# Performance work log

Measured on AMD Instinct MI355X. Metric: run time of the kernel, lower is better.

Reference implementation:

```python
import jax, jax.numpy as jnp
import numpy as np

B, C, H, W = 32, 256, 64, 64
LN_EPS = 1e-5

def _conv1x1(x, w, b=None):
    # x: (b,c,h,w), w: (out,c) -> (b,out,h,w)
    y = jnp.einsum('bchw,oc->bohw', x, w)
    if b is not None:
        y = y + b[None, :, None, None]
    return y

def _hsigmoid(t):
    # mmcv HSigmoid: clamp((x + 3) / 6, 0, 1)
    return jnp.clip((t + 3.0) / 6.0, 0.0, 1.0)

def setup_inputs() -> dict:
    key = jax.random.key(0)
    ks = jax.random.split(key, 12)
    s = 0.05
    return {
        'x': jax.random.normal(ks[0], (B, C, H, W), jnp.float32),
        'conv0_w': jax.random.normal(ks[1], (C // 2, C), jnp.float32) * s,
        'conv0_b': jnp.zeros((C // 2,), jnp.float32),
        'bn1_w': jax.random.normal(ks[2], (C, C // 2), jnp.float32) * s,
        'bn1_b': jnp.zeros((C,), jnp.float32),
        'conv1_w': jax.random.normal(ks[3], (1, C), jnp.float32) * s,
        'conv1_b': jnp.zeros((1,), jnp.float32),
        'ln_g': jnp.ones((C,), jnp.float32),
        'ln_b': jnp.zeros((C,), jnp.float32),
        'sk_w1': jax.random.normal(ks[4], (C // 2, C), jnp.float32) * s,
        'sk_w2': jax.random.normal(ks[5], (C, C // 2), jnp.float32) * s,
        'res_w': jax.random.normal(ks[6], (C, C), jnp.float32) * s,
        'res_b': jnp.zeros((C,), jnp.float32),
    }

def reference(x, conv0_w, conv0_b, bn1_w, bn1_b, conv1_w, conv1_b,
              ln_g, ln_b, sk_w1, sk_w2, res_w, res_b):
    b, c, h, w = x.shape
    # ---- channel attention ----
    ca = _conv1x1(x, conv0_w, conv0_b)               # (b, c/2, h, w)
    ca = ca.mean(axis=(2, 3), keepdims=True)          # GAP -> (b, c/2, 1, 1)
    ca = _conv1x1(ca, bn1_w, bn1_b)                   # (b, c, 1, 1)
    ca = _hsigmoid(ca)
    v = ca.reshape(b, c)                              # nchw_to_nlc -> (b, 1, c); LN over c
    mu = v.mean(axis=-1, keepdims=True)
    var = ((v - mu) ** 2).mean(axis=-1, keepdims=True)
    v = (v - mu) * jax.lax.rsqrt(var + LN_EPS) * ln_g + ln_b
    ca = v.reshape(b, c, 1, 1)
    # ---- spatial attention ----
    sa = _conv1x1(x, conv1_w, conv1_b)                # (b, 1, h, w)
    # ---- parallel attention ----
    par = _hsigmoid(sa + ca)                          # (b, c, h, w)
    # ---- sequence attention: bmm outer product (b,c,1)x(b,1,hw) ----
    seq = _hsigmoid(ca * sa)                          # (b, c, h, w)
    # ---- SK module ----
    u = (seq + par).mean(axis=(2, 3), keepdims=True)  # GAP -> (b, c, 1, 1)
    u = _conv1x1(u, sk_w1)                            # (b, c/2, 1, 1), no bias
    u = _conv1x1(u, sk_w2)                            # (b, c, 1, 1), no bias
    a = jax.nn.softmax(u, axis=1)
    sk = seq * a + par * (1.0 - a)
    # softmax over spatial (nchw_to_nlc + Softmax(dim=1))
    sk = jax.nn.softmax(sk.reshape(b, c, h * w), axis=2).reshape(b, c, h, w)
    selected = x * sk
    # ---- self attention ----
    self_attn = selected.sum(axis=(2, 3)).reshape(b, c, 1, 1) + _conv1x1(x, res_w, res_b)
    return selected + self_attn
```

## Files before the change

### kernel.cpp

```cpp
#include <hip/hip_runtime.h>
#include <math.h>

#define B_  32
#define C_  256
#define HW_ 4096
#define LN_EPS 1e-5f

typedef __attribute__((ext_vector_type(4))) float f32x4;
typedef __attribute__((ext_vector_type(8))) short bf16x8;

__device__ __forceinline__ float hsig(float v) {
    return fminf(fmaxf((v + 3.0f) * (1.0f / 6.0f), 0.0f), 1.0f);
}
__device__ __forceinline__ float tval(float ca, float a, float sav) {
    return a * hsig(ca * sav) + (1.0f - a) * hsig(ca + sav);
}
__device__ __forceinline__ unsigned short f2bf(float f) {
    unsigned u = __float_as_uint(f);
    unsigned r = (u + 0x7fffu + ((u >> 16) & 1u)) >> 16;
    return (unsigned short)r;
}
__device__ __forceinline__ float bf2f(unsigned short h) {
    return __uint_as_float(((unsigned)h) << 16);
}

__global__ void k_pass1(const float* __restrict__ x, const float* __restrict__ w1,
                        float* __restrict__ sa,
                        float* __restrict__ xs_part)
{
    int tid = threadIdx.x, wave = tid >> 6, lane = tid & 63;
    int hwq = blockIdx.x, b = blockIdx.y, ct = blockIdx.z;
    int c0 = ct * 32;
    int hw0 = hwq * 1024;
    const float* xb = x + (size_t)b * (C_ * HW_) + hw0 + tid * 4;
    __shared__ float part[32 * 4];
    f32x4 sacc = {0.f, 0.f, 0.f, 0.f};
    #pragma unroll 4
    for (int cc = 0; cc < 32; ++cc) {
        int c = c0 + cc;
        f32x4 v = *(const f32x4*)(xb + (size_t)c * HW_);
        float wv = w1[c];
        sacc += wv * v;
        float h = (v.x + v.y) + (v.z + v.w);
        h += __shfl_xor(h, 32); h += __shfl_xor(h, 16); h += __shfl_xor(h, 8);
        h += __shfl_xor(h, 4);  h += __shfl_xor(h, 2);  h += __shfl_xor(h, 1);
        if (lane == 0) part[cc * 4 + wave] = h;
    }
    float* sp = sa + (size_t)b * HW_ + hw0 + tid * 4;
    atomicAdd(sp + 0, sacc.x);
    atomicAdd(sp + 1, sacc.y);
    atomicAdd(sp + 2, sacc.z);
    atomicAdd(sp + 3, sacc.w);
    __syncthreads();
    if (tid < 32)
        xs_part[((size_t)hwq * B_ + b) * C_ + c0 + tid] =
            part[tid * 4 + 0] + part[tid * 4 + 1] + part[tid * 4 + 2] + part[tid * 4 + 3];
}

__global__ void k_ca(const float* __restrict__ xs_part, const float* __restrict__ w0,
                     const float* __restrict__ b0, const float* __restrict__ w1,
                     const float* __restrict__ b1, const float* __restrict__ g,
                     const float* __restrict__ be, float* __restrict__ ca,
                     const float* __restrict__ rw, unsigned short* __restrict__ wbs) {
    int b = blockIdx.x, tid = threadIdx.x;
    __shared__ float xm[C_], t0[128], red[4];
    float xs = xs_part[((size_t)0 * B_ + b) * C_ + tid]
             + xs_part[((size_t)1 * B_ + b) * C_ + tid]
             + xs_part[((size_t)2 * B_ + b) * C_ + tid]
             + xs_part[((size_t)3 * B_ + b) * C_ + tid];
    xm[tid] = xs * (1.0f / HW_);
    __syncthreads();
    if (tid < 128) {
        float s = b0[tid];
        const float* wr = w0 + tid * C_;
        for (int c = 0; c < C_; ++c) s += wr[c] * xm[c];
        t0[tid] = s;
    }
    __syncthreads();
    float s = b1[tid];
    const float* wr = w1 + tid * 128;
    for (int o = 0; o < 128; ++o) s += wr[o] * t0[o];
    float v = hsig(s);
    float sum = v;
    #pragma unroll
    for (int o = 32; o; o >>= 1) sum += __shfl_xor(sum, o);
    if ((tid & 63) == 0) red[tid >> 6] = sum;
    __syncthreads();
    float mu = (red[0] + red[1] + red[2] + red[3]) * (1.0f / C_);
    __syncthreads();
    float d = v - mu;
    float sq = d * d;
    #pragma unroll
    for (int o = 32; o; o >>= 1) sq += __shfl_xor(sq, o);
    if ((tid & 63) == 0) red[tid >> 6] = sq;
    __syncthreads();
    float var = (red[0] + red[1] + red[2] + red[3]) * (1.0f / C_);
    ca[b * C_ + tid] = d * (1.0f / sqrtf(var + LN_EPS)) * g[tid] + be[tid];

    int gid = b * 256 + tid;
    int lane = gid & 63;
    int mi = (gid >> 6) & 3;
    int ks = (gid >> 8) & 7;
    int wv2 = gid >> 11;
    int m = wv2 * 64 + mi * 16 + (lane & 15);
    int kb = ks * 32 + (lane >> 4) * 8;
    const float* src = rw + m * C_ + kb;
    f32x4 a4 = *(const f32x4*)src;
    f32x4 b4 = *(const f32x4*)(src + 4);
    ushort4 o0 = { f2bf(a4.x), f2bf(a4.y), f2bf(a4.z), f2bf(a4.w) };
    ushort4 o1 = { f2bf(b4.x), f2bf(b4.y), f2bf(b4.z), f2bf(b4.w) };
    unsigned short* dst = wbs + (size_t)gid * 8;
    *(ushort4*)dst = o0;
    *(ushort4*)(dst + 4) = o1;
}

__global__ void k_u(const float* __restrict__ sa, const float* __restrict__ ca,
                    const float* __restrict__ b1, float* __restrict__ u) {
    int bc = blockIdx.x;
    int b = bc >> 8;
    int tid = threadIdx.x;
    float cav = ca[bc];
    float bias = b1[0];
    const float* sp = sa + (size_t)b * HW_;
    float s = 0.f;
    for (int i = 0; i < 16; ++i) {
        f32x4 v = *(const f32x4*)(sp + i * 256 + tid * 4);
        #pragma unroll
        for (int j = 0; j < 4; ++j) {
            float sv = v[j] + bias;
            s += hsig(cav * sv) + hsig(cav + sv);
        }
    }
    #pragma unroll
    for (int o = 32; o; o >>= 1) s += __shfl_xor(s, o);
    if (tid == 0) u[bc] = s * (1.0f / HW_);
}

__global__ void k_a(const float* __restrict__ u, const float* __restrict__ w1,
                    const float* __restrict__ w2, float* __restrict__ aout) {
    int b = blockIdx.x, tid = threadIdx.x;
    __shared__ float uu[C_], v0[128], red[4];
    uu[tid] = u[b * C_ + tid];
    __syncthreads();
    if (tid < 128) {
        float s = 0.f;
        const float* wr = w1 + tid * C_;
        for (int c = 0; c < C_; ++c) s += wr[c] * uu[c];
        v0[tid] = s;
    }
    __syncthreads();
    float s = 0.f;
    const float* wr = w2 + tid * 128;
    for (int o = 0; o < 128; ++o) s += wr[o] * v0[o];
    float m = s;
    #pragma unroll
    for (int o = 32; o; o >>= 1) m = fmaxf(m, __shfl_xor(m, o));
    if ((tid & 63) == 0) red[tid >> 6] = m;
    __syncthreads();
    m = fmaxf(fmaxf(red[0], red[1]), fmaxf(red[2], red[3]));
    __syncthreads();
    float e = __expf(s - m);
    float se = e;
    #pragma unroll
    for (int o = 32; o; o >>= 1) se += __shfl_xor(se, o);
    if ((tid & 63) == 0) red[tid >> 6] = se;
    __syncthreads();
    float tot = red[0] + red[1] + red[2] + red[3];
    aout[b * C_ + tid] = e / tot;
}

__global__ void k_stats(const float* __restrict__ x, const float* __restrict__ sa,
                        const float* __restrict__ b1,
                        const float* __restrict__ ca, const float* __restrict__ aw,
                        const float* __restrict__ res_b, f32x4* __restrict__ st4) {
    int bc = blockIdx.x;
    int b = bc >> 8, c = bc & 255;
    int tid = threadIdx.x;
    float cav = ca[bc], av = aw[bc];
    float bias = b1[0];
    const float* sp = sa + (size_t)b * HW_;
    const float* xp = x + (size_t)bc * HW_;
    float se = 0.f, xe = 0.f;
    #pragma unroll
    for (int i = 0; i < 4; ++i) {
        f32x4 s4 = *(const f32x4*)(sp + i * 1024 + tid * 4);
        f32x4 x4 = *(const f32x4*)(xp + i * 1024 + tid * 4);
        #pragma unroll
        for (int j = 0; j < 4; ++j) {
            float e = __expf(tval(cav, av, s4[j] + bias));
            se += e;
            xe += x4[j] * e;
        }
    }
    __shared__ float red[4], red2[4];
    #pragma unroll
    for (int o = 32; o; o >>= 1) { se += __shfl_xor(se, o); xe += __shfl_xor(xe, o); }
    if ((tid & 63) == 0) { red[tid >> 6] = se; red2[tid >> 6] = xe; }
    __syncthreads();
    if (tid == 0) {
        float S = red[0] + red[1] + red[2] + red[3];
        float X = red2[0] + red2[1] + red2[2] + red2[3];
        float rcp = 1.0f / S;
        f32x4 st = { cav, av, rcp, X * rcp + res_b[c] };
        st4[bc] = st;
    }
}

__global__ __launch_bounds__(256, 2) void k_out(
    const float* __restrict__ x, const unsigned short* __restrict__ wbs,
    const float* __restrict__ sa, const float* __restrict__ b1,
    const f32x4* __restrict__ st4, float* __restrict__ out)
{
    __shared__ __align__(16) unsigned short Bs[64 * 256];
    __shared__ f32x4 sst[C_];
    __shared__ float ssa[64];

    int b = blockIdx.x, tile = blockIdx.y;
    int n0 = tile * 64;
    int tid = threadIdx.x;
    int w = tid >> 6, lane = tid & 63;

    const float* xb = x + (size_t)b * (C_ * HW_);

    bf16x8 af[8][4];
    #pragma unroll
    for (int ks = 0; ks < 8; ++ks)
        #pragma unroll
        for (int mi = 0; mi < 4; ++mi)
            af[ks][mi] = *(const bf16x8*)(wbs + (size_t)(((w * 8 + ks) * 4 + mi) * 64 + lane) * 8);

    sst[tid] = st4[b * C_ + tid];
    if (tid < 64) ssa[tid] = sa[(size_t)b * HW_ + n0 + tid] + b1[0];

    #pragma unroll
    for (int p2 = 0; p2 < 8; ++p2) {
        int id = p2 * 256 + tid;
        int kp = id >> 4;
        int tcn = id & 15;
        const float* g0 = xb + (size_t)(2 * kp) * HW_ + n0 + 4 * tcn;
        f32x4 v0 = *(const f32x4*)g0;
        f32x4 v1 = *(const f32x4*)(g0 + HW_);
        #pragma unroll
        for (int i = 0; i < 4; ++i) {
            int n = 4 * tcn + i;
            unsigned val = (unsigned)f2bf(v0[i]) | ((unsigned)f2bf(v1[i]) << 16);
            int bo = (n * 512 + kp * 4) ^ ((n & 7) << 4);
            *(unsigned*)((char*)Bs + bo) = val;
        }
    }
    __syncthreads();

    f32x4 acc[4][4];
    #pragma unroll
    for (int i = 0; i < 4; ++i)
        #pragma unroll
        for (int j = 0; j < 4; ++j) acc[i][j] = (f32x4){0.f, 0.f, 0.f, 0.f};

    #pragma unroll
    for (int ks = 0; ks < 8; ++ks) {
        bf16x8 bfr[4];
        #pragma unroll
        for (int ni = 0; ni < 4; ++ni) {
            int n = ni * 16 + (lane & 15);
            int bo = (n * 512 + ks * 64 + (lane >> 4) * 16) ^ ((n & 7) << 4);
            bfr[ni] = *(const bf16x8*)((const char*)Bs + bo);
        }
        #pragma unroll
        for (int mi = 0; mi < 4; ++mi)
            #pragma unroll
            for (int ni = 0; ni < 4; ++ni)
                acc[mi][ni] = __builtin_amdgcn_mfma_f32_16x16x32_bf16(
                    af[ks][mi], bfr[ni], acc[mi][ni], 0, 0, 0);
    }

    float* ob = out + (size_t)b * (C_ * HW_) + n0;
    #pragma unroll
    for (int mi = 0; mi < 4; ++mi) {
        int m0 = w * 64 + mi * 16 + (lane >> 4) * 4;
        f32x4 s0 = sst[m0 + 0];
        f32x4 s1 = sst[m0 + 1];
        f32x4 s2 = sst[m0 + 2];
        f32x4 s3 = sst[m0 + 3];
        #pragma unroll
        for (int ni = 0; ni < 4; ++ni) {
            int n = ni * 16 + (lane & 15);
            float sav = ssa[n];
            int bo = (n * 512 + m0 * 2) ^ ((n & 7) << 4);
            ushort4 xv = *(const ushort4*)((const char*)Bs + bo);
            float o0 = acc[mi][ni][0] + bf2f(xv.x) * (__expf(tval(s0.x, s0.y, sav)) * s0.z) + s0.w;
            float o1 = acc[mi][ni][1] + bf2f(xv.y) * (__expf(tval(s1.x, s1.y, sav)) * s1.z) + s1.w;
            float o2 = acc[mi][ni][2] + bf2f(xv.z) * (__expf(tval(s2.x, s2.y, sav)) * s2.z) + s2.w;
            float o3 = acc[mi][ni][3] + bf2f(xv.w) * (__expf(tval(s3.x, s3.y, sav)) * s3.z) + s3.w;
            ob[(size_t)(m0 + 0) * HW_ + n] = o0;
            ob[(size_t)(m0 + 1) * HW_ + n] = o1;
            ob[(size_t)(m0 + 2) * HW_ + n] = o2;
            ob[(size_t)(m0 + 3) * HW_ + n] = o3;
        }
    }
}

extern "C" void kernel_launch(void* const* d_in, const int* in_sizes, int n_in,
                              void* d_out, int out_size, void* d_ws, size_t ws_size,
                              hipStream_t stream) {
    (void)in_sizes; (void)n_in; (void)out_size; (void)ws_size;
    const float* x   = (const float*)d_in[0];
    const float* c0w = (const float*)d_in[1];
    const float* c0b = (const float*)d_in[2];
    const float* b1w = (const float*)d_in[3];
    const float* b1b = (const float*)d_in[4];
    const float* c1w = (const float*)d_in[5];
    const float* c1b = (const float*)d_in[6];
    const float* lng = (const float*)d_in[7];
    const float* lnb = (const float*)d_in[8];
    const float* sw1 = (const float*)d_in[9];
    const float* sw2 = (const float*)d_in[10];
    const float* rw  = (const float*)d_in[11];
    const float* rb  = (const float*)d_in[12];
    float* out = (float*)d_out;

    float* ws = (float*)d_ws;
    float* sa      = ws;
    float* xs_part = ws + 131072;
    float* ca      = ws + 163840;
    float* u       = ws + 172032;
    float* aw      = ws + 180224;
    f32x4* st4     = (f32x4*)(ws + 188416);
    unsigned short* wbs = (unsigned short*)(ws + 221184);

    hipMemsetAsync(sa, 0, (size_t)B_ * HW_ * sizeof(float), stream);
    hipLaunchKernelGGL(k_pass1, dim3(4, 32, 8), dim3(256), 0, stream, x, c1w, sa, xs_part);
    hipLaunchKernelGGL(k_ca,    dim3(32),       dim3(256), 0, stream, xs_part, c0w, c0b, b1w, b1b, lng, lnb, ca, rw, wbs);
    hipLaunchKernelGGL(k_u,     dim3(8192),     dim3(64),  0, stream, sa, ca, c1b, u);
    hipLaunchKernelGGL(k_a,     dim3(32),       dim3(256), 0, stream, u, sw1, sw2, aw);
    hipLaunchKernelGGL(k_stats, dim3(8192),     dim3(256), 0, stream, x, sa, c1b, ca, aw, rb, st4);
    hipLaunchKernelGGL(k_out,   dim3(32, 64),   dim3(256), 0, stream, x, wbs, sa, c1b, st4, out);
}
```

Before: 154.4 us.

## Write transposed bf16 copy of x in pass1 and read it in stats/out

```diff
diff --git a/kernel.cpp b/kernel.cpp
--- a/kernel.cpp
+++ b/kernel.cpp
@@ -8,6 +8,7 @@
 
 typedef __attribute__((ext_vector_type(4))) float f32x4;
 typedef __attribute__((ext_vector_type(8))) short bf16x8;
+typedef __attribute__((ext_vector_type(4))) unsigned u32x4;
 
 __device__ __forceinline__ float hsig(float v) {
     return fminf(fmaxf((v + 3.0f) * (1.0f / 6.0f), 0.0f), 1.0f);
@@ -24,9 +25,331 @@
     return __uint_as_float(((unsigned)h) << 16);
 }
 
+
+__global__ __launch_bounds__(256) void k_pass1t(
+    const float* __restrict__ x, const float* __restrict__ w1,
+    float* __restrict__ sa, float* __restrict__ xs_part,
+    unsigned short* __restrict__ xbf)
+{
+    __shared__ float sw1[C_];
+    __shared__ float xacc[32 * 257];
+    int b = blockIdx.x, hwc = blockIdx.y;
+    int tid = threadIdx.x;
+    int lane = tid & 63;
+    int grp = tid >> 3;
+    int hw = hwc * 256 + tid;
+    sw1[tid] = w1[tid];
+    __syncthreads();
+    const float* xb = x + (size_t)b * (C_ * HW_) + hw;
+    char* xrow = (char*)xbf + ((size_t)b * HW_ + hw) * 512;
+    float sacc = 0.f;
+    for (int cb = 0; cb < 4; ++cb) {
+        unsigned dwbuf[32];
+        #pragma unroll
+        for (int cg = 0; cg < 8; ++cg) {
+            int c = cb * 64 + cg * 8;
+            float v[8];
+            #pragma unroll
+            for (int j = 0; j < 8; ++j) v[j] = xb[(size_t)(c + j) * HW_];
+            float rr[8];
+            #pragma unroll
+            for (int j = 0; j < 8; ++j) {
+                sacc += sw1[c + j] * v[j];
+                float r = v[j];
+                r += __shfl_xor(r, 1); r += __shfl_xor(r, 2); r += __shfl_xor(r, 4);
+                rr[j] = r;
+            }
+            if ((lane & 7) == 0) {
+                #pragma unroll
+                for (int j = 0; j < 8; ++j) xacc[grp * 257 + c + j] = rr[j];
+            }
+            #pragma unroll
+            for (int j2 = 0; j2 < 4; ++j2)
+                dwbuf[cg * 4 + j2] = (unsigned)f2bf(v[2 * j2]) |
+                                     ((unsigned)f2bf(v[2 * j2 + 1]) << 16);
+        }
+        #pragma unroll
+        for (int q = 0; q < 8; ++q) {
+            u32x4 t = { dwbuf[q*4+0], dwbuf[q*4+1], dwbuf[q*4+2], dwbuf[q*4+3] };
+            *(u32x4*)(xrow + cb * 128 + q * 16) = t;
+        }
+    }
+    sa[(size_t)b * HW_ + hw] = sacc;
+    __syncthreads();
+    float s = 0.f;
+    #pragma unroll
+    for (int g = 0; g < 32; ++g) s += xacc[g * 257 + tid];
+    xs_part[((size_t)hwc * B_ + b) * C_ + tid] = s;
+}
+
+__global__ void k_ca(const float* __restrict__ xs_part, const float* __restrict__ w0,
+                     const float* __restrict__ b0, const float* __restrict__ w1,
+                     const float* __restrict__ b1, const float* __restrict__ g,
+                     const float* __restrict__ be, float* __restrict__ ca,
+                     const float* __restrict__ rw, unsigned short* __restrict__ wbs,
+                     int nparts) {
+    int b = blockIdx.x, tid = threadIdx.x;
+    __shared__ float xm[C_], t0[128], red[4];
+    float xs = 0.f;
+    for (int i = 0; i < nparts; ++i)
+        xs += xs_part[((size_t)i * B_ + b) * C_ + tid];
+    xm[tid] = xs * (1.0f / HW_);
+    __syncthreads();
+    if (tid < 128) {
+        float s = b0[tid];
+        const float* wr = w0 + tid * C_;
+        for (int c = 0; c < C_; ++c) s += wr[c] * xm[c];
+        t0[tid] = s;
+    }
+    __syncthreads();
+    float s = b1[tid];
+    const float* wr = w1 + tid * 128;
+    for (int o = 0; o < 128; ++o) s += wr[o] * t0[o];
+    float v = hsig(s);
+    float sum = v;
+    #pragma unroll
+    for (int o = 32; o; o >>= 1) sum += __shfl_xor(sum, o);
+    if ((tid & 63) == 0) red[tid >> 6] = sum;
+    __syncthreads();
+    float mu = (red[0] + red[1] + red[2] + red[3]) * (1.0f / C_);
+    __syncthreads();
+    float d = v - mu;
+    float sq = d * d;
+    #pragma unroll
+    for (int o = 32; o; o >>= 1) sq += __shfl_xor(sq, o);
+    if ((tid & 63) == 0) red[tid >> 6] = sq;
+    __syncthreads();
+    float var = (red[0] + red[1] + red[2] + red[3]) * (1.0f / C_);
+    ca[b * C_ + tid] = d * (1.0f / sqrtf(var + LN_EPS)) * g[tid] + be[tid];
+
+    int gid = b * 256 + tid;
+    int lane = gid & 63;
+    int mi = (gid >> 6) & 3;
+    int ks = (gid >> 8) & 7;
+    int wv2 = gid >> 11;
+    int m = wv2 * 64 + mi * 16 + (lane & 15);
+    int kb = ks * 32 + (lane >> 4) * 8;
+    const float* src = rw + m * C_ + kb;
+    f32x4 a4 = *(const f32x4*)src;
+    f32x4 b4 = *(const f32x4*)(src + 4);
+    ushort4 o0 = { f2bf(a4.x), f2bf(a4.y), f2bf(a4.z), f2bf(a4.w) };
+    ushort4 o1 = { f2bf(b4.x), f2bf(b4.y), f2bf(b4.z), f2bf(b4.w) };
+    unsigned short* dst = wbs + (size_t)gid * 8;
+    *(ushort4*)dst = o0;
+    *(ushort4*)(dst + 4) = o1;
+}
+
+__global__ void k_u(const float* __restrict__ sa, const float* __restrict__ ca,
+                    const float* __restrict__ b1, float* __restrict__ u) {
+    int bc = blockIdx.x;
+    int b = bc >> 8;
+    int tid = threadIdx.x;
+    float cav = ca[bc];
+    float bias = b1[0];
+    const float* sp = sa + (size_t)b * HW_;
+    float s = 0.f;
+    for (int i = 0; i < 16; ++i) {
+        f32x4 v = *(const f32x4*)(sp + i * 256 + tid * 4);
+        #pragma unroll
+        for (int j = 0; j < 4; ++j) {
+            float sv = v[j] + bias;
+            s += hsig(cav * sv) + hsig(cav + sv);
+        }
+    }
+    #pragma unroll
+    for (int o = 32; o; o >>= 1) s += __shfl_xor(s, o);
+    if (tid == 0) u[bc] = s * (1.0f / HW_);
+}
+
+__global__ void k_a(const float* __restrict__ u, const float* __restrict__ w1,
+                    const float* __restrict__ w2, float* __restrict__ aout) {
+    int b = blockIdx.x, tid = threadIdx.x;
+    __shared__ float uu[C_], v0[128], red[4];
+    uu[tid] = u[b * C_ + tid];
+    __syncthreads();
+    if (tid < 128) {
+        float s = 0.f;
+        const float* wr = w1 + tid * C_;
+        for (int c = 0; c < C_; ++c) s += wr[c] * uu[c];
+        v0[tid] = s;
+    }
+    __syncthreads();
+    float s = 0.f;
+    const float* wr = w2 + tid * 128;
+    for (int o = 0; o < 128; ++o) s += wr[o] * v0[o];
+    float m = s;
+    #pragma unroll
+    for (int o = 32; o; o >>= 1) m = fmaxf(m, __shfl_xor(m, o));
+    if ((tid & 63) == 0) red[tid >> 6] = m;
+    __syncthreads();
+    m = fmaxf(fmaxf(red[0], red[1]), fmaxf(red[2], red[3]));
+    __syncthreads();
+    float e = __expf(s - m);
+    float se = e;
+    #pragma unroll
+    for (int o = 32; o; o >>= 1) se += __shfl_xor(se, o);
+    if ((tid & 63) == 0) red[tid >> 6] = se;
+    __syncthreads();
+    float tot = red[0] + red[1] + red[2] + red[3];
+    aout[b * C_ + tid] = e / tot;
+}
+
+__global__ __launch_bounds__(512) void k_stats2(
+    const unsigned* __restrict__ xbf, const float* __restrict__ sa,
+    const float* __restrict__ b1, const float* __restrict__ ca,
+    const float* __restrict__ aw, const float* __restrict__ res_b,
+    f32x4* __restrict__ st4)
+{
+    __shared__ float ssa[HW_];
+    __shared__ float red[4 * 512];
+    int b = blockIdx.x, kpg = blockIdx.y;
+    int tid = threadIdx.x;
+    int kp_l = tid & 15, hwg = tid >> 4;
+    int kp = kpg * 16 + kp_l;
+    float bias = b1[0];
+    const float* sap = sa + (size_t)b * HW_;
+    #pragma unroll
+    for (int i = 0; i < 2; ++i) {
+        f32x4 v = *(const f32x4*)(sap + i * 2048 + tid * 4);
+        v.x += bias; v.y += bias; v.z += bias; v.w += bias;
+        *(f32x4*)(ssa + i * 2048 + tid * 4) = v;
+    }
+    int c0 = b * C_ + 2 * kp;
+    float ca0 = ca[c0], ca1 = ca[c0 + 1];
+    float a0 = aw[c0],  a1 = aw[c0 + 1];
+    __syncthreads();
+    const unsigned* xp = xbf + (size_t)b * (HW_ * 128) + kp;
+    float se0 = 0.f, xe0 = 0.f, se1 = 0.f, xe1 = 0.f;
+    #pragma unroll 4
+    for (int r = 0; r < 128; ++r) {
+        int hw = r * 32 + hwg;
+        unsigned v = xp[(size_t)hw * 128];
+        float sav = ssa[hw];
+        float e0 = __expf(tval(ca0, a0, sav));
+        float e1 = __expf(tval(ca1, a1, sav));
+        se0 += e0; se1 += e1;
+        xe0 += bf2f((unsigned short)(v & 0xffffu)) * e0;
+        xe1 += bf2f((unsigned short)(v >> 16)) * e1;
+    }
+    red[0 * 512 + hwg * 16 + kp_l] = se0;
+    red[1 * 512 + hwg * 16 + kp_l] = se1;
+    red[2 * 512 + hwg * 16 + kp_l] = xe0;
+    red[3 * 512 + hwg * 16 + kp_l] = xe1;
+    __syncthreads();
+    if (tid < 32) {
+        int kpl = tid & 15, hi = tid >> 4;
+        float se = 0.f, xe = 0.f;
+        #pragma unroll
+        for (int g = 0; g < 32; ++g) {
+            se += red[hi * 512 + g * 16 + kpl];
+            xe += red[(2 + hi) * 512 + g * 16 + kpl];
+        }
+        int c = kpg * 32 + 2 * kpl + hi;
+        int bc = b * C_ + c;
+        float rcp = 1.0f / se;
+        f32x4 st = { ca[bc], aw[bc], rcp, xe * rcp + res_b[c] };
+        st4[bc] = st;
+    }
+}
+
+__global__ __launch_bounds__(256, 3) void k_out2(
+    const unsigned short* __restrict__ xbf, const unsigned short* __restrict__ wbs,
+    const float* __restrict__ sa, const float* __restrict__ b1,
+    const f32x4* __restrict__ st4, float* __restrict__ out)
+{
+    __shared__ __align__(16) unsigned short Bs[64 * 256];
+    __shared__ f32x4 sst[C_];
+    __shared__ float ssa[64];
+
+    int b = blockIdx.x, tile = blockIdx.y;
+    int n0 = tile * 64;
+    int tid = threadIdx.x;
+    int w = tid >> 6, lane = tid & 63;
+
+    const char* src = (const char*)xbf + (((size_t)(b * 64 + tile)) << 15);
+    #pragma unroll
+    for (int p = 0; p < 8; ++p) {
+        int lbase = p * 4096 + w * 1024;
+        int off = lbase + lane * 16;
+        int soff = off ^ (((off >> 9) & 7) << 4);
+        __builtin_amdgcn_global_load_lds((const unsigned int*)(src + soff),
+                                         (unsigned int*)((char*)Bs + lbase), 16, 0, 0);
+    }
+
+    bf16x8 af[2][4];
+    const bf16x8* wp = (const bf16x8*)wbs;
+    #pragma unroll
+    for (int ks2 = 0; ks2 < 2; ++ks2)
+        #pragma unroll
+        for (int mi = 0; mi < 4; ++mi)
+            af[ks2][mi] = wp[(size_t)(((w * 8 + ks2) * 4 + mi) * 64 + lane)];
+
+    sst[tid] = st4[b * C_ + tid];
+    if (tid < 64) ssa[tid] = sa[(size_t)b * HW_ + n0 + tid] + b1[0];
+
+    __syncthreads();
+
+    f32x4 acc[4][4];
+    #pragma unroll
+    for (int i = 0; i < 4; ++i)
+        #pragma unroll
+        for (int j = 0; j < 4; ++j) acc[i][j] = (f32x4){0.f, 0.f, 0.f, 0.f};
+
+    #pragma unroll
+    for (int ksg = 0; ksg < 4; ++ksg) {
+        #pragma unroll
+        for (int ks2 = 0; ks2 < 2; ++ks2) {
+            int ks = ksg * 2 + ks2;
+            bf16x8 bfr[4];
+            #pragma unroll
+            for (int ni = 0; ni < 4; ++ni) {
+                int n = ni * 16 + (lane & 15);
+                int bo = (n * 512 + ks * 64 + (lane >> 4) * 16) ^ ((n & 7) << 4);
+                bfr[ni] = *(const bf16x8*)((const char*)Bs + bo);
+            }
+            #pragma unroll
+            for (int mi = 0; mi < 4; ++mi)
+                #pragma unroll
+                for (int ni = 0; ni < 4; ++ni)
+                    acc[mi][ni] = __builtin_amdgcn_mfma_f32_16x16x32_bf16(
+                        af[ks2][mi], bfr[ni], acc[mi][ni], 0, 0, 0);
+            if (ksg < 3) {
+                #pragma unroll
+                for (int mi = 0; mi < 4; ++mi)
+                    af[ks2][mi] = wp[(size_t)(((w * 8 + (ksg + 1) * 2 + ks2) * 4 + mi) * 64 + lane)];
+            }
+        }
+    }
+
+    float* ob = out + (size_t)b * (C_ * HW_) + n0;
+    #pragma unroll
+    for (int mi = 0; mi < 4; ++mi) {
+        int m0 = w * 64 + mi * 16 + (lane >> 4) * 4;
+        f32x4 s0 = sst[m0 + 0];
+        f32x4 s1 = sst[m0 + 1];
+        f32x4 s2 = sst[m0 + 2];
+        f32x4 s3 = sst[m0 + 3];
+        #pragma unroll
+        for (int ni = 0; ni < 4; ++ni) {
+            int n = ni * 16 + (lane & 15);
+            float sav = ssa[n];
+            int bo = (n * 512 + m0 * 2) ^ ((n & 7) << 4);
+            ushort4 xv = *(const ushort4*)((const char*)Bs + bo);
+            float o0 = acc[mi][ni][0] + bf2f(xv.x) * (__expf(tval(s0.x, s0.y, sav)) * s0.z) + s0.w;
+            float o1 = acc[mi][ni][1] + bf2f(xv.y) * (__expf(tval(s1.x, s1.y, sav)) * s1.z) + s1.w;
+            float o2 = acc[mi][ni][2] + bf2f(xv.z) * (__expf(tval(s2.x, s2.y, sav)) * s2.z) + s2.w;
+            float o3 = acc[mi][ni][3] + bf2f(xv.w) * (__expf(tval(s3.x, s3.y, sav)) * s3.z) + s3.w;
+            ob[(size_t)(m0 + 0) * HW_ + n] = o0;
+            ob[(size_t)(m0 + 1) * HW_ + n] = o1;
+            ob[(size_t)(m0 + 2) * HW_ + n] = o2;
+            ob[(size_t)(m0 + 3) * HW_ + n] = o3;
+        }
+    }
+}
+
+
 __global__ void k_pass1(const float* __restrict__ x, const float* __restrict__ w1,
-                        float* __restrict__ sa,
-                        float* __restrict__ xs_part)
+                        float* __restrict__ sa, float* __restrict__ xs_part)
 {
     int tid = threadIdx.x, wave = tid >> 6, lane = tid & 63;
     int hwq = blockIdx.x, b = blockIdx.y, ct = blockIdx.z;
@@ -57,118 +380,6 @@
             part[tid * 4 + 0] + part[tid * 4 + 1] + part[tid * 4 + 2] + part[tid * 4 + 3];
 }
 
-__global__ void k_ca(const float* __restrict__ xs_part, const float* __restrict__ w0,
-                     const float* __restrict__ b0, const float* __restrict__ w1,
-                     const float* __restrict__ b1, const float* __restrict__ g,
-                     const float* __restrict__ be, float* __restrict__ ca,
-                     const float* __restrict__ rw, unsigned short* __restrict__ wbs) {
-    int b = blockIdx.x, tid = threadIdx.x;
-    __shared__ float xm[C_], t0[128], red[4];
-    float xs = xs_part[((size_t)0 * B_ + b) * C_ + tid]
-             + xs_part[((size_t)1 * B_ + b) * C_ + tid]
-             + xs_part[((size_t)2 * B_ + b) * C_ + tid]
-             + xs_part[((size_t)3 * B_ + b) * C_ + tid];
-    xm[tid] = xs * (1.0f / HW_);
-    __syncthreads();
-    if (tid < 128) {
-        float s = b0[tid];
-        const float* wr = w0 + tid * C_;
-        for (int c = 0; c < C_; ++c) s += wr[c] * xm[c];
-        t0[tid] = s;
-    }
-    __syncthreads();
-    float s = b1[tid];
-    const float* wr = w1 + tid * 128;
-    for (int o = 0; o < 128; ++o) s += wr[o] * t0[o];
-    float v = hsig(s);
-    float sum = v;
-    #pragma unroll
-    for (int o = 32; o; o >>= 1) sum += __shfl_xor(sum, o);
-    if ((tid & 63) == 0) red[tid >> 6] = sum;
-    __syncthreads();
-    float mu = (red[0] + red[1] + red[2] + red[3]) * (1.0f / C_);
-    __syncthreads();
-    float d = v - mu;
-    float sq = d * d;
-    #pragma unroll
-    for (int o = 32; o; o >>= 1) sq += __shfl_xor(sq, o);
-    if ((tid & 63) == 0) red[tid >> 6] = sq;
-    __syncthreads();
-    float var = (red[0] + red[1] + red[2] + red[3]) * (1.0f / C_);
-    ca[b * C_ + tid] = d * (1.0f / sqrtf(var + LN_EPS)) * g[tid] + be[tid];
-
-    int gid = b * 256 + tid;
-    int lane = gid & 63;
-    int mi = (gid >> 6) & 3;
-    int ks = (gid >> 8) & 7;
-    int wv2 = gid >> 11;
-    int m = wv2 * 64 + mi * 16 + (lane & 15);
-    int kb = ks * 32 + (lane >> 4) * 8;
-    const float* src = rw + m * C_ + kb;
-    f32x4 a4 = *(const f32x4*)src;
-    f32x4 b4 = *(const f32x4*)(src + 4);
-    ushort4 o0 = { f2bf(a4.x), f2bf(a4.y), f2bf(a4.z), f2bf(a4.w) };
-    ushort4 o1 = { f2bf(b4.x), f2bf(b4.y), f2bf(b4.z), f2bf(b4.w) };
-    unsigned short* dst = wbs + (size_t)gid * 8;
-    *(ushort4*)dst = o0;
-    *(ushort4*)(dst + 4) = o1;
-}
-
-__global__ void k_u(const float* __restrict__ sa, const float* __restrict__ ca,
-                    const float* __restrict__ b1, float* __restrict__ u) {
-    int bc = blockIdx.x;
-    int b = bc >> 8;
-    int tid = threadIdx.x;
-    float cav = ca[bc];
-    float bias = b1[0];
-    const float* sp = sa + (size_t)b * HW_;
-    float s = 0.f;
-    for (int i = 0; i < 16; ++i) {
-        f32x4 v = *(const f32x4*)(sp + i * 256 + tid * 4);
-        #pragma unroll
-        for (int j = 0; j < 4; ++j) {
-            float sv = v[j] + bias;
-            s += hsig(cav * sv) + hsig(cav + sv);
-        }
-    }
-    #pragma unroll
-    for (int o = 32; o; o >>= 1) s += __shfl_xor(s, o);
-    if (tid == 0) u[bc] = s * (1.0f / HW_);
-}
-
-__global__ void k_a(const float* __restrict__ u, const float* __restrict__ w1,
-                    const float* __restrict__ w2, float* __restrict__ aout) {
-    int b = blockIdx.x, tid = threadIdx.x;
-    __shared__ float uu[C_], v0[128], red[4];
-    uu[tid] = u[b * C_ + tid];
-    __syncthreads();
-    if (tid < 128) {
-        float s = 0.f;
-        const float* wr = w1 + tid * C_;
-        for (int c = 0; c < C_; ++c) s += wr[c] * uu[c];
-        v0[tid] = s;
-    }
-    __syncthreads();
-    float s = 0.f;
-    const float* wr = w2 + tid * 128;
-    for (int o = 0; o < 128; ++o) s += wr[o] * v0[o];
-    float m = s;
-    #pragma unroll
-    for (int o = 32; o; o >>= 1) m = fmaxf(m, __shfl_xor(m, o));
-    if ((tid & 63) == 0) red[tid >> 6] = m;
-    __syncthreads();
-    m = fmaxf(fmaxf(red[0], red[1]), fmaxf(red[2], red[3]));
-    __syncthreads();
-    float e = __expf(s - m);
-    float se = e;
-    #pragma unroll
-    for (int o = 32; o; o >>= 1) se += __shfl_xor(se, o);
-    if ((tid & 63) == 0) red[tid >> 6] = se;
-    __syncthreads();
-    float tot = red[0] + red[1] + red[2] + red[3];
-    aout[b * C_ + tid] = e / tot;
-}
-
 __global__ void k_stats(const float* __restrict__ x, const float* __restrict__ sa,
                         const float* __restrict__ b1,
                         const float* __restrict__ ca, const float* __restrict__ aw,
@@ -302,7 +513,7 @@
 extern "C" void kernel_launch(void* const* d_in, const int* in_sizes, int n_in,
                               void* d_out, int out_size, void* d_ws, size_t ws_size,
                               hipStream_t stream) {
-    (void)in_sizes; (void)n_in; (void)out_size; (void)ws_size;
+    (void)in_sizes; (void)n_in; (void)out_size;
     const float* x   = (const float*)d_in[0];
     const float* c0w = (const float*)d_in[1];
     const float* c0b = (const float*)d_in[2];
@@ -317,21 +528,40 @@
     const float* rw  = (const float*)d_in[11];
     const float* rb  = (const float*)d_in[12];
     float* out = (float*)d_out;
-
     float* ws = (float*)d_ws;
-    float* sa      = ws;
-    float* xs_part = ws + 131072;
-    float* ca      = ws + 163840;
-    float* u       = ws + 172032;
-    float* aw      = ws + 180224;
-    f32x4* st4     = (f32x4*)(ws + 188416);
-    unsigned short* wbs = (unsigned short*)(ws + 221184);
-
-    hipMemsetAsync(sa, 0, (size_t)B_ * HW_ * sizeof(float), stream);
-    hipLaunchKernelGGL(k_pass1, dim3(4, 32, 8), dim3(256), 0, stream, x, c1w, sa, xs_part);
-    hipLaunchKernelGGL(k_ca,    dim3(32),       dim3(256), 0, stream, xs_part, c0w, c0b, b1w, b1b, lng, lnb, ca, rw, wbs);
-    hipLaunchKernelGGL(k_u,     dim3(8192),     dim3(64),  0, stream, sa, ca, c1b, u);
-    hipLaunchKernelGGL(k_a,     dim3(32),       dim3(256), 0, stream, u, sw1, sw2, aw);
-    hipLaunchKernelGGL(k_stats, dim3(8192),     dim3(256), 0, stream, x, sa, c1b, ca, aw, rb, st4);
-    hipLaunchKernelGGL(k_out,   dim3(32, 64),   dim3(256), 0, stream, x, wbs, sa, c1b, st4, out);
-}
+
+    const size_t NEW_WS_FLOATS = (size_t)352256 + 16777216;
+    if (ws_size >= NEW_WS_FLOATS * sizeof(float)) {
+        float* sa      = ws;
+        float* xs_part = ws + 131072;
+        float* ca      = ws + 262144;
+        float* u       = ws + 270336;
+        float* aw      = ws + 278528;
+        f32x4* st4     = (f32x4*)(ws + 286720);
+        unsigned short* wbs = (unsigned short*)(ws + 319488);
+        unsigned short* xbf = (unsigned short*)(ws + 352256);
+
+        hipLaunchKernelGGL(k_pass1t, dim3(32, 16), dim3(256), 0, stream, x, c1w, sa, xs_part, xbf);
+        hipLaunchKernelGGL(k_ca,     dim3(32),     dim3(256), 0, stream, xs_part, c0w, c0b, b1w, b1b, lng, lnb, ca, rw, wbs, 16);
+        hipLaunchKernelGGL(k_u,      dim3(8192),   dim3(64),  0, stream, sa, ca, c1b, u);
+        hipLaunchKernelGGL(k_a,      dim3(32),     dim3(256), 0, stream, u, sw1, sw2, aw);
+        hipLaunchKernelGGL(k_stats2, dim3(32, 8),  dim3(512), 0, stream, (const unsigned*)xbf, sa, c1b, ca, aw, rb, st4);
+        hipLaunchKernelGGL(k_out2,   dim3(32, 64), dim3(256), 0, stream, xbf, wbs, sa, c1b, st4, out);
+    } else {
+        float* sa      = ws;
+        float* xs_part = ws + 131072;
+        float* ca      = ws + 163840;
+        float* u       = ws + 172032;
+        float* aw      = ws + 180224;
+        f32x4* st4     = (f32x4*)(ws + 188416);
+        unsigned short* wbs = (unsigned short*)(ws + 221184);
+
+        hipMemsetAsync(sa, 0, (size_t)B_ * HW_ * sizeof(float), stream);
+        hipLaunchKernelGGL(k_pass1, dim3(4, 32, 8), dim3(256), 0, stream, x, c1w, sa, xs_part);
+        hipLaunchKernelGGL(k_ca,    dim3(32),       dim3(256), 0, stream, xs_part, c0w, c0b, b1w, b1b, lng, lnb, ca, rw, wbs, 4);
+        hipLaunchKernelGGL(k_u,     dim3(8192),     dim3(64),  0, stream, sa, ca, c1b, u);
+        hipLaunchKernelGGL(k_a,     dim3(32),       dim3(256), 0, stream, u, sw1, sw2, aw);
+        hipLaunchKernelGGL(k_stats, dim3(8192),     dim3(256), 0, stream, x, sa, c1b, ca, aw, rb, st4);
+        hipLaunchKernelGGL(k_out,   dim3(32, 64),   dim3(256), 0, stream, x, wbs, sa, c1b, st4, out);
+    }
+}
```

Measured after the change: 179.8 us. 16.5% more time.
